# Performance work log

Measured on AMD Instinct MI355X. Metric: run time of the kernel, lower is better.

Reference implementation:

```python
import jax, jax.numpy as jnp
import numpy as np

SEQ, EMB, QKV = 4096, 1024, 1024

def setup_inputs() -> dict:
    key = jax.random.key(0)
    k_x, k_q, k_k, k_v = jax.random.split(key, 4)
    scale = 1.0 / np.sqrt(EMB)
    return {
        "x": jax.random.normal(k_x, (SEQ, EMB), dtype=jnp.float32),
        "W_q": jax.random.normal(k_q, (EMB, QKV), dtype=jnp.float32) * scale,
        "W_k": jax.random.normal(k_k, (EMB, QKV), dtype=jnp.float32) * scale,
        "W_v": jax.random.normal(k_v, (EMB, QKV), dtype=jnp.float32) * scale,
    }

def reference(x, W_q, W_k, W_v):
    # Single-head scaled dot-product attention, unbatched: x [S, E]
    d_k = W_q.shape[1]
    Q = x @ W_q          # [S, D]
    K = x @ W_k          # [S, D]
    V = x @ W_v          # [S, D]
    scores = (Q @ K.T) * (1.0 / jnp.sqrt(jnp.asarray(d_k, dtype=x.dtype)))  # [S, S]
    attn = jax.nn.softmax(scores, axis=-1)
    return attn @ V      # [S, D]
```

## Files before the change

kernel.cpp:

```cpp
#include <hip/hip_runtime.h>
#include <cstdint>

#define S_DIM 4096
#define E_DIM 1024
#define D_DIM 1024

typedef __bf16 bf16x8 __attribute__((ext_vector_type(8)));
typedef float  f32x4  __attribute__((ext_vector_type(4)));
typedef unsigned short u16x8 __attribute__((ext_vector_type(8)));

__device__ __forceinline__ unsigned short f2bf(float f) {
  unsigned u = __float_as_uint(f);
  unsigned r = (u + 0x7fffu + ((u >> 16) & 1u)) >> 16;
  return (unsigned short)r;
}
__device__ __forceinline__ unsigned short to_bf16_bits(float f) { return f2bf(f); }
__device__ __forceinline__ unsigned short to_bf16_bits(unsigned short s) { return s; }

__device__ __forceinline__ void lds_copy16(const unsigned short* g, const unsigned short* l) {
  auto gp = reinterpret_cast<__attribute__((address_space(1))) unsigned int*>(
      reinterpret_cast<uintptr_t>(g));
  auto lp = reinterpret_cast<__attribute__((address_space(3))) unsigned int*>(
      reinterpret_cast<uintptr_t>(l));
  __builtin_amdgcn_global_load_lds(gp, lp, 16, 0, 0);
}

__global__ __launch_bounds__(256) void cvt_f32_bf16_kernel(
    const float* __restrict__ in, unsigned short* __restrict__ out, int n) {
  int i = (blockIdx.x * 256 + threadIdx.x) * 8;
  if (i >= n) return;
  float4 a = *(const float4*)(in + i);
  float4 b = *(const float4*)(in + i + 4);
  u16x8 o;
  o[0] = f2bf(a.x); o[1] = f2bf(a.y); o[2] = f2bf(a.z); o[3] = f2bf(a.w);
  o[4] = f2bf(b.x); o[5] = f2bf(b.y); o[6] = f2bf(b.z); o[7] = f2bf(b.w);
  *(u16x8*)(out + i) = o;
}

template <typename TIN>
__global__ __launch_bounds__(256) void transpose_to_bf16_kernel(
    const TIN* __restrict__ in, unsigned short* __restrict__ out, int ldin, int ldout) {
  __shared__ unsigned short tile[32][33];
  int bc = blockIdx.x * 32, br = blockIdx.y * 32;
  int tx = threadIdx.x & 31;
  int ty = threadIdx.x >> 5;
#pragma unroll
  for (int i = 0; i < 32; i += 8)
    tile[ty + i][tx] = to_bf16_bits(in[(size_t)(br + ty + i) * ldin + bc + tx]);
  __syncthreads();
#pragma unroll
  for (int i = 0; i < 32; i += 8)
    out[(size_t)(bc + ty + i) * ldout + br + tx] = tile[tx][ty + i];
}

template <int MODE, bool SPLIT3>
__global__ __launch_bounds__(256, 2) void gemm_bt_kernel(
    const unsigned short* __restrict__ A, int lda,
    const unsigned short* __restrict__ Bt, int ldb,
    void* __restrict__ Cp, unsigned short* __restrict__ C1,
    unsigned short* __restrict__ C2, int ldc,
    int Kper, float scale, float* __restrict__ lsum) {
  __shared__ __align__(16) unsigned short sA[128 * 32];
  __shared__ __align__(16) unsigned short sB[128 * 32];

  const int tid = threadIdx.x;

  int flat = blockIdx.y * gridDim.x + blockIdx.x;
  int numInG = 8 * gridDim.x;
  int g = flat / numInG;
  int r = flat - g * numInG;
  const int bm = (g * 8 + (r & 7)) * 128;
  const int bn = (r >> 3) * 128;

  const int wave = tid >> 6;
  const int lane = tid & 63;
  const int q    = lane >> 4;
  const int l16  = lane & 15;
  const int wm   = (wave >> 1) * 64;
  const int wn   = (wave & 1) * 64;

  f32x4 zero = {0.f, 0.f, 0.f, 0.f};
  f32x4 acc[4][4];
#pragma unroll
  for (int t = 0; t < 4; t++)
#pragma unroll
    for (int u = 0; u < 4; u++) acc[t][u] = zero;

  const int srow   = tid >> 2;
  const int schunk = (tid & 3) ^ (srow & 3);
  const int kbase  = blockIdx.z * Kper;
  const unsigned short* ap = A  + (size_t)(bm + srow) * lda + kbase + schunk * 8;
  const unsigned short* bp = Bt + (size_t)(bn + srow) * ldb + kbase + schunk * 8;
  unsigned short* saw = sA + wave * 512;
  unsigned short* sbw = sB + wave * 512;
  const size_t skipA = (size_t)64 * lda;
  const size_t skipB = (size_t)64 * ldb;

  const int sw = (q ^ (l16 & 3)) * 8;

  for (int k0 = 0; k0 < Kper; k0 += 32) {
    lds_copy16(ap + k0,         saw);
    lds_copy16(ap + k0 + skipA, saw + 2048);
    lds_copy16(bp + k0,         sbw);
    lds_copy16(bp + k0 + skipB, sbw + 2048);
    __syncthreads();

    bf16x8 af[4], bfv[4];
#pragma unroll
    for (int t = 0; t < 4; t++)
      af[t] = *reinterpret_cast<const bf16x8*>(sA + (wm + t * 16 + l16) * 32 + sw);
#pragma unroll
    for (int u = 0; u < 4; u++)
      bfv[u] = *reinterpret_cast<const bf16x8*>(sB + (wn + u * 16 + l16) * 32 + sw);
#pragma unroll
    for (int t = 0; t < 4; t++)
#pragma unroll
      for (int u = 0; u < 4; u++)
        acc[t][u] = __builtin_amdgcn_mfma_f32_16x16x32_bf16(af[t], bfv[u], acc[t][u], 0, 0, 0);
    __syncthreads();
  }

  unsigned short* cb16 = (unsigned short*)Cp;
  int coloff = bn;
  if constexpr (SPLIT3) {
    int which = bn >> 10;
    cb16 = (which == 0) ? (unsigned short*)Cp : (which == 1 ? C1 : C2);
    coloff = bn & 1023;
  }

#pragma unroll
  for (int t = 0; t < 4; t++) {
#pragma unroll
    for (int rr = 0; rr < 4; rr++) {
      const int row = bm + wm + t * 16 + q * 4 + rr;
      float invl = 1.0f;
      if constexpr (MODE == 2) invl = 1.0f / lsum[row];
      float rs = 0.f;
#pragma unroll
      for (int u = 0; u < 4; u++) {
        const int col = coloff + wn + u * 16 + l16;
        float v = acc[t][u][rr] * scale;
        if constexpr (MODE == 0) {
          cb16[(size_t)row * ldc + col] = f2bf(v);
        } else if constexpr (MODE == 1) {
          float p = __expf(v - 8.0f);
          rs += p;
          cb16[(size_t)row * ldc + col] = f2bf(p);
        } else {
          unsafeAtomicAdd((float*)Cp + (size_t)row * ldc + col, acc[t][u][rr] * invl);
        }
      }
      if constexpr (MODE == 1) {
        rs += __shfl_xor(rs, 1);
        rs += __shfl_xor(rs, 2);
        rs += __shfl_xor(rs, 4);
        rs += __shfl_xor(rs, 8);
        if (l16 == 0) unsafeAtomicAdd(&lsum[row], rs);
      }
    }
  }
}

extern "C" void kernel_launch(void* const* d_in, const int* in_sizes, int n_in,
                              void* d_out, int out_size, void* d_ws, size_t ws_size,
                              hipStream_t stream) {
  const float* x  = (const float*)d_in[0];
  const float* Wq = (const float*)d_in[1];
  const float* Wk = (const float*)d_in[2];
  const float* Wv = (const float*)d_in[3];
  float* out = (float*)d_out;

  char* ws = (char*)d_ws;
  const size_t MB = 1024 * 1024;
  unsigned short* SP   = (unsigned short*)(ws);
  unsigned short* Vtmp = (unsigned short*)(ws);
  unsigned short* xbf  = (unsigned short*)(ws + 8 * MB);
  unsigned short* Wt   = (unsigned short*)(ws + 16 * MB);
  unsigned short* Qbf  = (unsigned short*)(ws + 32 * MB);
  unsigned short* Kbf  = (unsigned short*)(ws + 40 * MB);
  unsigned short* Vt   = (unsigned short*)(ws + 48 * MB);
  float*          lsum = (float*)(ws + 56 * MB);

  dim3 blk(256);

  cvt_f32_bf16_kernel<<<(S_DIM * E_DIM) / (256 * 8), blk, 0, stream>>>(x, xbf, S_DIM * E_DIM);

  dim3 tgrid(32, 32);
  transpose_to_bf16_kernel<float><<<tgrid, blk, 0, stream>>>(Wq, Wt,                   D_DIM, E_DIM);
  transpose_to_bf16_kernel<float><<<tgrid, blk, 0, stream>>>(Wk, Wt + 1024 * 1024,     D_DIM, E_DIM);
  transpose_to_bf16_kernel<float><<<tgrid, blk, 0, stream>>>(Wv, Wt + 2 * 1024 * 1024, D_DIM, E_DIM);

  dim3 pgrid(24, 32, 1);
  gemm_bt_kernel<0, true><<<pgrid, blk, 0, stream>>>(
      xbf, E_DIM, Wt, E_DIM, Qbf, Kbf, Vtmp, D_DIM, E_DIM, 1.0f, nullptr);

  dim3 vtgrid(32, 128);
  transpose_to_bf16_kernel<unsigned short><<<vtgrid, blk, 0, stream>>>(Vtmp, Vt, D_DIM, S_DIM);

  hipMemsetAsync(lsum, 0, S_DIM * sizeof(float), stream);
  dim3 sgrid(32, 32, 1);
  gemm_bt_kernel<1, false><<<sgrid, blk, 0, stream>>>(
      Qbf, D_DIM, Kbf, D_DIM, SP, nullptr, nullptr, S_DIM, D_DIM, 0.03125f, lsum);

  hipMemsetAsync(out, 0, (size_t)S_DIM * D_DIM * sizeof(float), stream);
  dim3 ogrid(8, 32, 2);
  gemm_bt_kernel<2, false><<<ogrid, blk, 0, stream>>>(
      SP, S_DIM, Vt, S_DIM, out, nullptr, nullptr, D_DIM, S_DIM / 2, 1.0f, lsum);
}
```

Baseline: 246.3 us.

## Fuse input prep kernels and double GEMM K-tile to 64

The x conversion, the three weight transposes and the lsum memset are merged into a single prep kernel indexed by blockIdx.z, which removes several launches. The shared GEMM kernel now stages a 64-wide K slice per iteration (32KB of LDS per block) and runs two MFMA sub-steps between barriers, halving the number of __syncthreads and loop iterations. This raises LDS use per block and register pressure from the unrolled loads, which could limit occupancy.

```diff
diff --git a/kernel.cpp b/kernel.cpp
--- a/kernel.cpp
+++ b/kernel.cpp
@@ -14,8 +14,6 @@
   unsigned r = (u + 0x7fffu + ((u >> 16) & 1u)) >> 16;
   return (unsigned short)r;
 }
-__device__ __forceinline__ unsigned short to_bf16_bits(float f) { return f2bf(f); }
-__device__ __forceinline__ unsigned short to_bf16_bits(unsigned short s) { return s; }
 
 __device__ __forceinline__ void lds_copy16(const unsigned short* g, const unsigned short* l) {
   auto gp = reinterpret_cast<__attribute__((address_space(1))) unsigned int*>(
@@ -25,28 +23,51 @@
   __builtin_amdgcn_global_load_lds(gp, lp, 16, 0, 0);
 }
 
-__global__ __launch_bounds__(256) void cvt_f32_bf16_kernel(
-    const float* __restrict__ in, unsigned short* __restrict__ out, int n) {
-  int i = (blockIdx.x * 256 + threadIdx.x) * 8;
-  if (i >= n) return;
-  float4 a = *(const float4*)(in + i);
-  float4 b = *(const float4*)(in + i + 4);
-  u16x8 o;
-  o[0] = f2bf(a.x); o[1] = f2bf(a.y); o[2] = f2bf(a.z); o[3] = f2bf(a.w);
-  o[4] = f2bf(b.x); o[5] = f2bf(b.y); o[6] = f2bf(b.z); o[7] = f2bf(b.w);
-  *(u16x8*)(out + i) = o;
-}
-
-template <typename TIN>
-__global__ __launch_bounds__(256) void transpose_to_bf16_kernel(
-    const TIN* __restrict__ in, unsigned short* __restrict__ out, int ldin, int ldout) {
+__global__ __launch_bounds__(256) void prep_kernel(
+    const float* __restrict__ x,
+    const float* __restrict__ Wq, const float* __restrict__ Wk, const float* __restrict__ Wv,
+    unsigned short* __restrict__ xbf, unsigned short* __restrict__ Wt,
+    float* __restrict__ lsum) {
+  const int z = blockIdx.z;
+  const int tid = threadIdx.x;
+  if (z < 3) {
+    const float* W = (z == 0) ? Wq : (z == 1 ? Wk : Wv);
+    unsigned short* out = Wt + (size_t)z * E_DIM * D_DIM;
+    __shared__ unsigned short tile[32][33];
+    int bc = blockIdx.x * 32, br = blockIdx.y * 32;
+    int tx = tid & 31, ty = tid >> 5;
+#pragma unroll
+    for (int i = 0; i < 32; i += 8)
+      tile[ty + i][tx] = f2bf(W[(size_t)(br + ty + i) * D_DIM + bc + tx]);
+    __syncthreads();
+#pragma unroll
+    for (int i = 0; i < 32; i += 8)
+      out[(size_t)(bc + ty + i) * E_DIM + br + tx] = tile[tx][ty + i];
+  } else {
+    int bid = blockIdx.y * 32 + blockIdx.x;
+    int i = (bid * 256 + tid) * 16;
+#pragma unroll
+    for (int h = 0; h < 2; h++) {
+      float4 a = *(const float4*)(x + i + h * 8);
+      float4 b = *(const float4*)(x + i + h * 8 + 4);
+      u16x8 o;
+      o[0] = f2bf(a.x); o[1] = f2bf(a.y); o[2] = f2bf(a.z); o[3] = f2bf(a.w);
+      o[4] = f2bf(b.x); o[5] = f2bf(b.y); o[6] = f2bf(b.z); o[7] = f2bf(b.w);
+      *(u16x8*)(xbf + i + h * 8) = o;
+    }
+    if (bid < 16) lsum[bid * 256 + tid] = 0.f;
+  }
+}
+
+__global__ __launch_bounds__(256) void transpose_bf16_kernel(
+    const unsigned short* __restrict__ in, unsigned short* __restrict__ out,
+    int ldin, int ldout) {
   __shared__ unsigned short tile[32][33];
   int bc = blockIdx.x * 32, br = blockIdx.y * 32;
-  int tx = threadIdx.x & 31;
-  int ty = threadIdx.x >> 5;
+  int tx = threadIdx.x & 31, ty = threadIdx.x >> 5;
 #pragma unroll
   for (int i = 0; i < 32; i += 8)
-    tile[ty + i][tx] = to_bf16_bits(in[(size_t)(br + ty + i) * ldin + bc + tx]);
+    tile[ty + i][tx] = in[(size_t)(br + ty + i) * ldin + bc + tx];
   __syncthreads();
 #pragma unroll
   for (int i = 0; i < 32; i += 8)
@@ -60,8 +81,8 @@
     void* __restrict__ Cp, unsigned short* __restrict__ C1,
     unsigned short* __restrict__ C2, int ldc,
     int Kper, float scale, float* __restrict__ lsum) {
-  __shared__ __align__(16) unsigned short sA[128 * 32];
-  __shared__ __align__(16) unsigned short sB[128 * 32];
+  __shared__ __align__(16) unsigned short sA[128 * 64];
+  __shared__ __align__(16) unsigned short sB[128 * 64];
 
   const int tid = threadIdx.x;
 
@@ -86,37 +107,41 @@
 #pragma unroll
     for (int u = 0; u < 4; u++) acc[t][u] = zero;
 
-  const int srow   = tid >> 2;
-  const int schunk = (tid & 3) ^ (srow & 3);
+  const int srow   = tid >> 3;
+  const int schunk = (tid & 7) ^ (srow & 3);
   const int kbase  = blockIdx.z * Kper;
   const unsigned short* ap = A  + (size_t)(bm + srow) * lda + kbase + schunk * 8;
   const unsigned short* bp = Bt + (size_t)(bn + srow) * ldb + kbase + schunk * 8;
   unsigned short* saw = sA + wave * 512;
   unsigned short* sbw = sB + wave * 512;
-  const size_t skipA = (size_t)64 * lda;
-  const size_t skipB = (size_t)64 * ldb;
+  const size_t stepA = (size_t)32 * lda;
+  const size_t stepB = (size_t)32 * ldb;
 
   const int sw = (q ^ (l16 & 3)) * 8;
 
-  for (int k0 = 0; k0 < Kper; k0 += 32) {
-    lds_copy16(ap + k0,         saw);
-    lds_copy16(ap + k0 + skipA, saw + 2048);
-    lds_copy16(bp + k0,         sbw);
-    lds_copy16(bp + k0 + skipB, sbw + 2048);
+  for (int k0 = 0; k0 < Kper; k0 += 64) {
+#pragma unroll
+    for (int p = 0; p < 4; p++) {
+      lds_copy16(ap + k0 + p * stepA, saw + p * 2048);
+      lds_copy16(bp + k0 + p * stepB, sbw + p * 2048);
+    }
     __syncthreads();
 
-    bf16x8 af[4], bfv[4];
-#pragma unroll
-    for (int t = 0; t < 4; t++)
-      af[t] = *reinterpret_cast<const bf16x8*>(sA + (wm + t * 16 + l16) * 32 + sw);
-#pragma unroll
-    for (int u = 0; u < 4; u++)
-      bfv[u] = *reinterpret_cast<const bf16x8*>(sB + (wn + u * 16 + l16) * 32 + sw);
-#pragma unroll
-    for (int t = 0; t < 4; t++)
+#pragma unroll
+    for (int h = 0; h < 2; h++) {
+      bf16x8 af[4], bfv[4];
+#pragma unroll
+      for (int t = 0; t < 4; t++)
+        af[t] = *reinterpret_cast<const bf16x8*>(sA + (wm + t * 16 + l16) * 64 + h * 32 + sw);
 #pragma unroll
       for (int u = 0; u < 4; u++)
-        acc[t][u] = __builtin_amdgcn_mfma_f32_16x16x32_bf16(af[t], bfv[u], acc[t][u], 0, 0, 0);
+        bfv[u] = *reinterpret_cast<const bf16x8*>(sB + (wn + u * 16 + l16) * 64 + h * 32 + sw);
+#pragma unroll
+      for (int t = 0; t < 4; t++)
+#pragma unroll
+        for (int u = 0; u < 4; u++)
+          acc[t][u] = __builtin_amdgcn_mfma_f32_16x16x32_bf16(af[t], bfv[u], acc[t][u], 0, 0, 0);
+    }
     __syncthreads();
   }
 
@@ -183,21 +208,16 @@
 
   dim3 blk(256);
 
-  cvt_f32_bf16_kernel<<<(S_DIM * E_DIM) / (256 * 8), blk, 0, stream>>>(x, xbf, S_DIM * E_DIM);
-
-  dim3 tgrid(32, 32);
-  transpose_to_bf16_kernel<float><<<tgrid, blk, 0, stream>>>(Wq, Wt,                   D_DIM, E_DIM);
-  transpose_to_bf16_kernel<float><<<tgrid, blk, 0, stream>>>(Wk, Wt + 1024 * 1024,     D_DIM, E_DIM);
-  transpose_to_bf16_kernel<float><<<tgrid, blk, 0, stream>>>(Wv, Wt + 2 * 1024 * 1024, D_DIM, E_DIM);
+  dim3 prgrid(32, 32, 4);
+  prep_kernel<<<prgrid, blk, 0, stream>>>(x, Wq, Wk, Wv, xbf, Wt, lsum);
 
   dim3 pgrid(24, 32, 1);
   gemm_bt_kernel<0, true><<<pgrid, blk, 0, stream>>>(
       xbf, E_DIM, Wt, E_DIM, Qbf, Kbf, Vtmp, D_DIM, E_DIM, 1.0f, nullptr);
 
   dim3 vtgrid(32, 128);
-  transpose_to_bf16_kernel<unsigned short><<<vtgrid, blk, 0, stream>>>(Vtmp, Vt, D_DIM, S_DIM);
-
-  hipMemsetAsync(lsum, 0, S_DIM * sizeof(float), stream);
+  transpose_bf16_kernel<<<vtgrid, blk, 0, stream>>>(Vtmp, Vt, D_DIM, S_DIM);
+
   dim3 sgrid(32, 32, 1);
   gemm_bt_kernel<1, false><<<sgrid, blk, 0, stream>>>(
       Qbf, D_DIM, Kbf, D_DIM, SP, nullptr, nullptr, S_DIM, D_DIM, 0.03125f, lsum);
```

Measured after the change: 228.1 us. 7.4% less time.
